# Kernel optimization log

Measured on AMD Instinct MI355X. Metric: run time of the kernel, lower is better.

## Reference

```python
import jax, jax.numpy as jnp
import numpy as np


def setup_inputs() -> dict:
    key = jax.random.key(0)
    k1, k2, k3, k4, k5 = jax.random.split(key, 5)
    C, Cr = 512, 64  # in_channels, in_channels // 8
    B, W, H = 16, 64, 64
    x = jax.random.normal(k1, (B, C, W, H), dtype=jnp.float32)
    # 1x1 conv == pointwise linear over channels; store as [out, in]
    w1 = jax.random.normal(k2, (Cr, C), dtype=jnp.float32) * (1.0 / np.sqrt(C))
    b1 = jax.random.normal(k3, (Cr,), dtype=jnp.float32) * 0.01
    w2 = jax.random.normal(k4, (C, Cr), dtype=jnp.float32) * (1.0 / np.sqrt(Cr))
    b2 = jax.random.normal(k5, (C,), dtype=jnp.float32) * 0.01
    return {"x": x, "w1": w1, "b1": b1, "w2": w2, "b2": b2}


def reference(x, w1, b1, w2, b2):
    B, C, W, H = x.shape
    # conv1x1: channel reduction C -> C//8
    r = jnp.einsum('bchw,oc->bohw', x, w1) + b1[None, :, None, None]
    q = r.reshape(B, -1, W * H)                      # [B, C', N] query/key/value
    # channel-channel attention map [B, C', C'] (bmm(query, key^T))
    att = jnp.einsum('bcn,bdn->bcd', q, q)
    att = jax.nn.softmax(att, axis=-1)
    out = jnp.einsum('bcd,bdn->bcn', att, q)          # [B, C', N]
    out = out.reshape(B, -1, W, H)
    # conv_out: channel expansion C//8 -> C, plus residual
    out = jnp.einsum('bchw,oc->bohw', out, w2) + b2[None, :, None, None]
    return out + x
```

## Files before the change

### kernel.cpp

```cpp
#include <hip/hip_runtime.h>
#include <math.h>

#define NPIX 4096
#define CIN  512
#define CR   64
#define NB   16
#define NCHUNK 32

typedef __bf16 bf16x8 __attribute__((ext_vector_type(8)));
typedef float  f32x4  __attribute__((ext_vector_type(4)));
typedef unsigned int uint;
typedef uint   uint4v __attribute__((ext_vector_type(4)));
typedef unsigned short ushort;

static const size_t W1B_OFF = 0;
static const size_t Q_OFF   = W1B_OFF + 65536;
static const size_t QT_OFF  = Q_OFF  + (size_t)NB*CR*NPIX*2;
static const size_t AP_OFF  = QT_OFF + (size_t)NB*NPIX*CR*2;
static const size_t ATT_OFF = AP_OFF + (size_t)NB*NCHUNK*CR*CR*4;
static const size_t MB_OFF  = ATT_OFF + (size_t)NB*CR*CR*4;

static __device__ inline uint pk_bf16(float a, float b) {
    uint r;
    asm volatile("v_cvt_pk_bf16_f32 %0, %1, %2" : "=v"(r) : "v"(a), "v"(b));
    return r;
}

__global__ __launch_bounds__(256) void k0_cast(const float* __restrict__ w1,
                                               uint* __restrict__ w1b) {
    int i = blockIdx.x * 256 + threadIdx.x;
    w1b[i] = pk_bf16(w1[2 * i], w1[2 * i + 1]);
}

__global__ __launch_bounds__(256) void k1_conv1(const float* __restrict__ x,
                                                const ushort* __restrict__ w1b,
                                                const float* __restrict__ b1,
                                                ushort* __restrict__ q,
                                                ushort* __restrict__ qt) {
    int b = blockIdx.y;
    int t = threadIdx.x;
    int wid = t >> 6, l = t & 63;
    int lo = l & 15, kg = l >> 4;
    int px0 = blockIdx.x * 256 + wid * 64;
    const float* xb = x + (size_t)b * CIN * NPIX;

    f32x4 acc[4][4] = {};
    for (int ks = 0; ks < 16; ks++) {
        int k0 = ks * 32 + kg * 8;
        float xv[4][8];
#pragma unroll
        for (int pf = 0; pf < 4; pf++) {
            const float* xp = xb + (size_t)k0 * NPIX + px0 + pf * 16 + lo;
#pragma unroll
            for (int j = 0; j < 8; j++) xv[pf][j] = xp[(size_t)j * NPIX];
        }
        bf16x8 af[4];
#pragma unroll
        for (int of = 0; of < 4; of++)
            af[of] = *(const bf16x8*)(w1b + (size_t)(of * 16 + lo) * CIN + k0);
#pragma unroll
        for (int pf = 0; pf < 4; pf++) {
            uint4v bu;
#pragma unroll
            for (int j = 0; j < 4; j++) bu[j] = pk_bf16(xv[pf][2 * j], xv[pf][2 * j + 1]);
            bf16x8 bf = __builtin_bit_cast(bf16x8, bu);
#pragma unroll
            for (int of = 0; of < 4; of++)
                acc[pf][of] = __builtin_amdgcn_mfma_f32_16x16x32_bf16(af[of], bf, acc[pf][of], 0, 0, 0);
        }
    }
#pragma unroll
    for (int pf = 0; pf < 4; pf++) {
        int px = px0 + pf * 16 + lo;
        ushort* qb  = q  + (size_t)b * CR * NPIX + px;
        ushort* qtb = qt + ((size_t)b * NPIX + px) * CR;
#pragma unroll
        for (int of = 0; of < 4; of++) {
            int o = of * 16 + kg * 4;
            float v0 = acc[pf][of][0] + b1[o + 0];
            float v1 = acc[pf][of][1] + b1[o + 1];
            float v2 = acc[pf][of][2] + b1[o + 2];
            float v3 = acc[pf][of][3] + b1[o + 3];
            uint p0 = pk_bf16(v0, v1), p1 = pk_bf16(v2, v3);
            qb[(size_t)(o + 0) * NPIX] = (ushort)(p0 & 0xffff);
            qb[(size_t)(o + 1) * NPIX] = (ushort)(p0 >> 16);
            qb[(size_t)(o + 2) * NPIX] = (ushort)(p1 & 0xffff);
            qb[(size_t)(o + 3) * NPIX] = (ushort)(p1 >> 16);
            *(uint2*)(qtb + o) = make_uint2(p0, p1);
        }
    }
}

__global__ __launch_bounds__(256) void k2a_att_part(const ushort* __restrict__ q,
                                                    float* __restrict__ ap) {
    int b = blockIdx.y;
    int ch = blockIdx.x * 4 + (threadIdx.x >> 6);
    int l = threadIdx.x & 63;
    int lo = l & 15, kg = l >> 4;
    const ushort* qb = q + (size_t)b * CR * NPIX + ch * 128;
    f32x4 acc[4][4] = {};
#pragma unroll
    for (int ks = 0; ks < 4; ks++) {
        bf16x8 fr[4];
#pragma unroll
        for (int cf = 0; cf < 4; cf++)
            fr[cf] = *(const bf16x8*)(qb + (size_t)(cf * 16 + lo) * NPIX + ks * 32 + kg * 8);
#pragma unroll
        for (int cf = 0; cf < 4; cf++)
#pragma unroll
            for (int df = 0; df < 4; df++)
                acc[cf][df] = __builtin_amdgcn_mfma_f32_16x16x32_bf16(fr[cf], fr[df], acc[cf][df], 0, 0, 0);
    }
    float* app = ap + ((size_t)(b * NCHUNK + ch) * CR) * CR;
#pragma unroll
    for (int cf = 0; cf < 4; cf++)
#pragma unroll
        for (int df = 0; df < 4; df++)
#pragma unroll
            for (int r = 0; r < 4; r++)
                app[(size_t)(cf * 16 + kg * 4 + r) * CR + df * 16 + lo] = acc[cf][df][r];
}

__global__ __launch_bounds__(256) void k2b_softmax(const float* __restrict__ ap,
                                                   float* __restrict__ att) {
    int cq = blockIdx.x, b = blockIdx.y;
    int t = threadIdx.x;
    int lane = t & 63;
    int c = cq * 4 + (t >> 6);
    float v = 0.f;
#pragma unroll 8
    for (int ch = 0; ch < NCHUNK; ch++)
        v += ap[(((size_t)(b * NCHUNK + ch) * CR) + c) * CR + lane];
    float m = v;
#pragma unroll
    for (int s = 1; s < 64; s <<= 1) m = fmaxf(m, __shfl_xor(m, s, 64));
    float e = __expf(v - m);
    float ssum = e;
#pragma unroll
    for (int s = 1; s < 64; s <<= 1) ssum += __shfl_xor(ssum, s, 64);
    att[((size_t)b * CR + c) * CR + lane] = e / ssum;
}

__global__ __launch_bounds__(256) void k3_m(const float* __restrict__ w2,
                                            const float* __restrict__ att,
                                            ushort* __restrict__ mb) {
    int b = blockIdx.y;
    int c = blockIdx.x * 256 + threadIdx.x;
    const float* ab  = att + (size_t)b * CR * CR;
    const float* w2r = w2 + (size_t)c * CR;
    float acc[CR];
#pragma unroll
    for (int d = 0; d < CR; d++) acc[d] = 0.f;
    for (int k = 0; k < CR; k++) {
        float wv = w2r[k];
#pragma unroll
        for (int d = 0; d < CR; d++) acc[d] = fmaf(wv, ab[k * CR + d], acc[d]);
    }
    uint* mp = (uint*)(mb + ((size_t)b * CIN + c) * CR);
#pragma unroll
    for (int i = 0; i < 8; i++) {
        uint4v u;
#pragma unroll
        for (int j = 0; j < 4; j++)
            u[j] = pk_bf16(acc[i * 8 + 2 * j], acc[i * 8 + 2 * j + 1]);
        *(uint4v*)(mp + i * 4) = u;
    }
}

__global__ __launch_bounds__(256) void k4_out(const ushort* __restrict__ qt,
                                              const ushort* __restrict__ mb,
                                              const float* __restrict__ b2,
                                              const float* __restrict__ x,
                                              float* __restrict__ y) {
    int cc = blockIdx.x, b = blockIdx.z;
    int t = threadIdx.x;
    int wid = t >> 6, l = t & 63;
    int lo = l & 15, kg = l >> 4;
    int px0 = blockIdx.y * 128 + wid * 32;
    int pxA = px0 + lo, pxB = px0 + 16 + lo;
    const ushort* qpA = qt + ((size_t)b * NPIX + pxA) * CR;
    const ushort* qpB = qt + ((size_t)b * NPIX + pxB) * CR;
    const ushort* mp = mb + ((size_t)b * CIN + cc * 64) * CR;

    bf16x8 bqA0 = *(const bf16x8*)(qpA + kg * 8);
    bf16x8 bqA1 = *(const bf16x8*)(qpA + 32 + kg * 8);
    bf16x8 bqB0 = *(const bf16x8*)(qpB + kg * 8);
    bf16x8 bqB1 = *(const bf16x8*)(qpB + 32 + kg * 8);
    bf16x8 am[4][2];
#pragma unroll
    for (int cf = 0; cf < 4; cf++) {
        am[cf][0] = *(const bf16x8*)(mp + (size_t)(cf * 16 + lo) * CR + kg * 8);
        am[cf][1] = *(const bf16x8*)(mp + (size_t)(cf * 16 + lo) * CR + 32 + kg * 8);
    }
    float xrA[4][4], xrB[4][4];
#pragma unroll
    for (int cf = 0; cf < 4; cf++)
#pragma unroll
        for (int r = 0; r < 4; r++) {
            size_t row = ((size_t)b * CIN + cc * 64 + cf * 16 + kg * 4 + r) * NPIX;
            xrA[cf][r] = x[row + pxA];
            xrB[cf][r] = x[row + pxB];
        }

    f32x4 accA[4] = {}, accB[4] = {};
#pragma unroll
    for (int cf = 0; cf < 4; cf++) {
        accA[cf] = __builtin_amdgcn_mfma_f32_16x16x32_bf16(am[cf][0], bqA0, accA[cf], 0, 0, 0);
        accA[cf] = __builtin_amdgcn_mfma_f32_16x16x32_bf16(am[cf][1], bqA1, accA[cf], 0, 0, 0);
        accB[cf] = __builtin_amdgcn_mfma_f32_16x16x32_bf16(am[cf][0], bqB0, accB[cf], 0, 0, 0);
        accB[cf] = __builtin_amdgcn_mfma_f32_16x16x32_bf16(am[cf][1], bqB1, accB[cf], 0, 0, 0);
    }
#pragma unroll
    for (int cf = 0; cf < 4; cf++) {
        int c = cc * 64 + cf * 16 + kg * 4;
#pragma unroll
        for (int r = 0; r < 4; r++) {
            size_t row = ((size_t)b * CIN + c + r) * NPIX;
            y[row + pxA] = accA[cf][r] + b2[c + r] + xrA[cf][r];
            y[row + pxB] = accB[cf][r] + b2[c + r] + xrB[cf][r];
        }
    }
}

extern "C" void kernel_launch(void* const* d_in, const int* in_sizes, int n_in,
                              void* d_out, int out_size, void* d_ws, size_t ws_size,
                              hipStream_t stream) {
    const float* x  = (const float*)d_in[0];
    const float* w1 = (const float*)d_in[1];
    const float* b1 = (const float*)d_in[2];
    const float* w2 = (const float*)d_in[3];
    const float* b2 = (const float*)d_in[4];
    float* y = (float*)d_out;
    char* ws = (char*)d_ws;

    uint*   w1b = (uint*)  (ws + W1B_OFF);
    ushort* q   = (ushort*)(ws + Q_OFF);
    ushort* qt  = (ushort*)(ws + QT_OFF);
    float*  ap  = (float*) (ws + AP_OFF);
    float*  att = (float*) (ws + ATT_OFF);
    ushort* mb  = (ushort*)(ws + MB_OFF);

    hipLaunchKernelGGL(k0_cast,     dim3(64),         dim3(256), 0, stream, w1, w1b);
    hipLaunchKernelGGL(k1_conv1,    dim3(16, 16),     dim3(256), 0, stream, x, (const ushort*)w1b, b1, q, qt);
    hipLaunchKernelGGL(k2a_att_part,dim3(8, 16),      dim3(256), 0, stream, q, ap);
    hipLaunchKernelGGL(k2b_softmax, dim3(16, 16),     dim3(256), 0, stream, ap, att);
    hipLaunchKernelGGL(k3_m,        dim3(2, 16),      dim3(256), 0, stream, w2, att, mb);
    hipLaunchKernelGGL(k4_out,      dim3(8, 32, 16),  dim3(256), 0, stream, qt, mb, b2, x, y);
}
```

Before: 125.6 us.

## Fuse attention partial sums and softmax via LDS; split k3 over output columns

The attention-partial and softmax kernels become one kernel per batch. Eight waves each accumulate a 512-pixel slice, reduce through shared memory, and apply the softmax directly, which removes the global partial buffer and one launch. Separately, k3_m is split four ways across the d dimension with vectorized loads, giving more blocks and fewer registers per thread. The tradeoff is that the fused attention kernel runs only 16 blocks, so it uses few CUs and each wave does a longer serial MFMA loop.

```diff
diff --git a/kernel.cpp b/kernel.cpp
--- a/kernel.cpp
+++ b/kernel.cpp
@@ -5,7 +5,6 @@
 #define CIN  512
 #define CR   64
 #define NB   16
-#define NCHUNK 32
 
 typedef __bf16 bf16x8 __attribute__((ext_vector_type(8)));
 typedef float  f32x4  __attribute__((ext_vector_type(4)));
@@ -16,8 +15,7 @@
 static const size_t W1B_OFF = 0;
 static const size_t Q_OFF   = W1B_OFF + 65536;
 static const size_t QT_OFF  = Q_OFF  + (size_t)NB*CR*NPIX*2;
-static const size_t AP_OFF  = QT_OFF + (size_t)NB*NPIX*CR*2;
-static const size_t ATT_OFF = AP_OFF + (size_t)NB*NCHUNK*CR*CR*4;
+static const size_t ATT_OFF = QT_OFF + (size_t)NB*NPIX*CR*2;
 static const size_t MB_OFF  = ATT_OFF + (size_t)NB*CR*CR*4;
 
 static __device__ inline uint pk_bf16(float a, float b) {
@@ -91,16 +89,17 @@
     }
 }
 
-__global__ __launch_bounds__(256) void k2a_att_part(const ushort* __restrict__ q,
-                                                    float* __restrict__ ap) {
-    int b = blockIdx.y;
-    int ch = blockIdx.x * 4 + (threadIdx.x >> 6);
-    int l = threadIdx.x & 63;
+__global__ __launch_bounds__(512) void k2_att(const ushort* __restrict__ q,
+                                              float* __restrict__ att) {
+    __shared__ float part[8][64][66];
+    int b = blockIdx.x;
+    int t = threadIdx.x;
+    int w = t >> 6, l = t & 63;
     int lo = l & 15, kg = l >> 4;
-    const ushort* qb = q + (size_t)b * CR * NPIX + ch * 128;
+    const ushort* qb = q + (size_t)b * CR * NPIX + w * 512;
+
     f32x4 acc[4][4] = {};
-#pragma unroll
-    for (int ks = 0; ks < 4; ks++) {
+    for (int ks = 0; ks < 16; ks++) {
         bf16x8 fr[4];
 #pragma unroll
         for (int cf = 0; cf < 4; cf++)
@@ -111,60 +110,57 @@
             for (int df = 0; df < 4; df++)
                 acc[cf][df] = __builtin_amdgcn_mfma_f32_16x16x32_bf16(fr[cf], fr[df], acc[cf][df], 0, 0, 0);
     }
-    float* app = ap + ((size_t)(b * NCHUNK + ch) * CR) * CR;
 #pragma unroll
     for (int cf = 0; cf < 4; cf++)
 #pragma unroll
         for (int df = 0; df < 4; df++)
 #pragma unroll
             for (int r = 0; r < 4; r++)
-                app[(size_t)(cf * 16 + kg * 4 + r) * CR + df * 16 + lo] = acc[cf][df][r];
-}
-
-__global__ __launch_bounds__(256) void k2b_softmax(const float* __restrict__ ap,
-                                                   float* __restrict__ att) {
-    int cq = blockIdx.x, b = blockIdx.y;
-    int t = threadIdx.x;
-    int lane = t & 63;
-    int c = cq * 4 + (t >> 6);
-    float v = 0.f;
-#pragma unroll 8
-    for (int ch = 0; ch < NCHUNK; ch++)
-        v += ap[(((size_t)(b * NCHUNK + ch) * CR) + c) * CR + lane];
-    float m = v;
-#pragma unroll
-    for (int s = 1; s < 64; s <<= 1) m = fmaxf(m, __shfl_xor(m, s, 64));
-    float e = __expf(v - m);
-    float ssum = e;
-#pragma unroll
-    for (int s = 1; s < 64; s <<= 1) ssum += __shfl_xor(ssum, s, 64);
-    att[((size_t)b * CR + c) * CR + lane] = e / ssum;
+                part[w][cf * 16 + kg * 4 + r][df * 16 + lo] = acc[cf][df][r];
+    __syncthreads();
+
+#pragma unroll
+    for (int i = 0; i < 8; i++) {
+        int c = w * 8 + i;
+        float v = 0.f;
+#pragma unroll
+        for (int pw = 0; pw < 8; pw++) v += part[pw][c][l];
+        float m = v;
+#pragma unroll
+        for (int s = 1; s < 64; s <<= 1) m = fmaxf(m, __shfl_xor(m, s, 64));
+        float e = __expf(v - m);
+        float ssum = e;
+#pragma unroll
+        for (int s = 1; s < 64; s <<= 1) ssum += __shfl_xor(ssum, s, 64);
+        att[((size_t)b * CR + c) * CR + l] = e / ssum;
+    }
 }
 
 __global__ __launch_bounds__(256) void k3_m(const float* __restrict__ w2,
                                             const float* __restrict__ att,
                                             ushort* __restrict__ mb) {
     int b = blockIdx.y;
-    int c = blockIdx.x * 256 + threadIdx.x;
-    const float* ab  = att + (size_t)b * CR * CR;
+    int c  = (blockIdx.x >> 2) * 256 + threadIdx.x;
+    int dg = (blockIdx.x & 3) * 16;
+    const float* ab  = att + (size_t)b * CR * CR + dg;
     const float* w2r = w2 + (size_t)c * CR;
-    float acc[CR];
-#pragma unroll
-    for (int d = 0; d < CR; d++) acc[d] = 0.f;
+    float acc[16];
+#pragma unroll
+    for (int j = 0; j < 16; j++) acc[j] = 0.f;
     for (int k = 0; k < CR; k++) {
         float wv = w2r[k];
 #pragma unroll
-        for (int d = 0; d < CR; d++) acc[d] = fmaf(wv, ab[k * CR + d], acc[d]);
-    }
-    uint* mp = (uint*)(mb + ((size_t)b * CIN + c) * CR);
-#pragma unroll
-    for (int i = 0; i < 8; i++) {
-        uint4v u;
-#pragma unroll
-        for (int j = 0; j < 4; j++)
-            u[j] = pk_bf16(acc[i * 8 + 2 * j], acc[i * 8 + 2 * j + 1]);
-        *(uint4v*)(mp + i * 4) = u;
-    }
+        for (int j4 = 0; j4 < 4; j4++) {
+            f32x4 av = *(const f32x4*)(ab + k * CR + j4 * 4);
+#pragma unroll
+            for (int u = 0; u < 4; u++)
+                acc[j4 * 4 + u] = fmaf(wv, av[u], acc[j4 * 4 + u]);
+        }
+    }
+    uint* mp = (uint*)(mb + ((size_t)b * CIN + c) * CR + dg);
+#pragma unroll
+    for (int i = 0; i < 8; i++)
+        mp[i] = pk_bf16(acc[2 * i], acc[2 * i + 1]);
 }
 
 __global__ __launch_bounds__(256) void k4_out(const ushort* __restrict__ qt,
@@ -236,14 +232,12 @@
     uint*   w1b = (uint*)  (ws + W1B_OFF);
     ushort* q   = (ushort*)(ws + Q_OFF);
     ushort* qt  = (ushort*)(ws + QT_OFF);
-    float*  ap  = (float*) (ws + AP_OFF);
     float*  att = (float*) (ws + ATT_OFF);
     ushort* mb  = (ushort*)(ws + MB_OFF);
 
-    hipLaunchKernelGGL(k0_cast,     dim3(64),         dim3(256), 0, stream, w1, w1b);
-    hipLaunchKernelGGL(k1_conv1,    dim3(16, 16),     dim3(256), 0, stream, x, (const ushort*)w1b, b1, q, qt);
-    hipLaunchKernelGGL(k2a_att_part,dim3(8, 16),      dim3(256), 0, stream, q, ap);
-    hipLaunchKernelGGL(k2b_softmax, dim3(16, 16),     dim3(256), 0, stream, ap, att);
-    hipLaunchKernelGGL(k3_m,        dim3(2, 16),      dim3(256), 0, stream, w2, att, mb);
-    hipLaunchKernelGGL(k4_out,      dim3(8, 32, 16),  dim3(256), 0, stream, qt, mb, b2, x, y);
-}
+    hipLaunchKernelGGL(k0_cast,  dim3(64),         dim3(256), 0, stream, w1, w1b);
+    hipLaunchKernelGGL(k1_conv1, dim3(16, 16),     dim3(256), 0, stream, x, (const ushort*)w1b, b1, q, qt);
+    hipLaunchKernelGGL(k2_att,   dim3(16),         dim3(512), 0, stream, q, att);
+    hipLaunchKernelGGL(k3_m,     dim3(8, 16),      dim3(256), 0, stream, w2, att, mb);
+    hipLaunchKernelGGL(k4_out,   dim3(8, 32, 16),  dim3(256), 0, stream, qt, mb, b2, x, y);
+}
```

After: 118.5 us. -5.6%, faster.
